# Performance work log

Measured on AMD Instinct MI355X. Metric: run time of the kernel, lower is better.

The kernel has to match this reference:

```python
import jax, jax.numpy as jnp
import numpy as np

IN, H = 23, 64


def _lstm_layer(x, W_ih, W_hh, b_ih, b_hh):
    # x: [B,T,in] ; W_ih: [4H,in] ; W_hh: [4H,H] ; gate order (PyTorch): i,f,g,o
    B = x.shape[0]
    # precompute input contribution for all timesteps (one big GEMM)
    xg = jnp.einsum('bti,gi->btg', x, W_ih) + (b_ih + b_hh)  # [B,T,4H]

    def step(carry, xt):
        h, c = carry
        gates = xt + h @ W_hh.T  # [B,4H]
        i, f, g, o = jnp.split(gates, 4, axis=-1)
        c = jax.nn.sigmoid(f) * c + jax.nn.sigmoid(i) * jnp.tanh(g)
        h = jax.nn.sigmoid(o) * jnp.tanh(c)
        return (h, c), h

    h0 = jnp.zeros((B, H), x.dtype)
    _, hs = jax.lax.scan(step, (h0, h0), jnp.swapaxes(xg, 0, 1))
    return jnp.swapaxes(hs, 0, 1)  # [B,T,H]


def setup_inputs() -> dict:
    key = jax.random.key(0)
    ks = jax.random.split(key, 12)
    s = 1.0 / np.sqrt(H)  # PyTorch LSTM init scale
    x = jax.random.normal(ks[0], (2048, 512, IN), dtype=jnp.float32)
    W_ih0 = jax.random.uniform(ks[1], (4 * H, IN), jnp.float32, -s, s)
    W_hh0 = jax.random.uniform(ks[2], (4 * H, H), jnp.float32, -s, s)
    b_ih0 = jax.random.uniform(ks[3], (4 * H,), jnp.float32, -s, s)
    b_hh0 = jax.random.uniform(ks[4], (4 * H,), jnp.float32, -s, s)
    W_ih1 = jax.random.uniform(ks[5], (4 * H, H), jnp.float32, -s, s)
    W_hh1 = jax.random.uniform(ks[6], (4 * H, H), jnp.float32, -s, s)
    b_ih1 = jax.random.uniform(ks[7], (4 * H,), jnp.float32, -s, s)
    b_hh1 = jax.random.uniform(ks[8], (4 * H,), jnp.float32, -s, s)
    fc_w = jax.random.uniform(ks[9], (1, H), jnp.float32, -s, s)
    fc_b = jax.random.uniform(ks[10], (1,), jnp.float32, -s, s)
    return {"x": x, "W_ih0": W_ih0, "W_hh0": W_hh0, "b_ih0": b_ih0, "b_hh0": b_hh0,
            "W_ih1": W_ih1, "W_hh1": W_hh1, "b_ih1": b_ih1, "b_hh1": b_hh1,
            "fc_w": fc_w, "fc_b": fc_b}


def reference(x, W_ih0, W_hh0, b_ih0, b_hh0, W_ih1, W_hh1, b_ih1, b_hh1, fc_w, fc_b):
    h1 = _lstm_layer(x, W_ih0, W_hh0, b_ih0, b_hh0)   # [B,T,H]
    h2 = _lstm_layer(h1, W_ih1, W_hh1, b_ih1, b_hh1)  # [B,T,H]
    last = h2[:, -1, :]                               # [B,H]
    return last @ fc_w.T + fc_b                       # [B,1]
```

## Files before the change

kernel.cpp:

```cpp
#include <hip/hip_runtime.h>

typedef _Float16 half8 __attribute__((ext_vector_type(8)));
typedef float floatx4 __attribute__((ext_vector_type(4)));

#define NSTEPS 512
#define IN_F   23
#define HSTRIDE 72

__device__ __forceinline__ float fast_rcp(float x) { return __builtin_amdgcn_rcpf(x); }
__device__ __forceinline__ float fast_sigmoid(float x) { return fast_rcp(1.f + __expf(-x)); }
__device__ __forceinline__ float fast_tanh(float x) { return 2.f * fast_rcp(1.f + __expf(-2.f * x)) - 1.f; }

#define MFMA3(acc, Ahi, Alo, Bhi, Blo)                                             \
    acc = __builtin_amdgcn_mfma_f32_16x16x32_f16((Ahi), (Bhi), (acc), 0, 0, 0);    \
    acc = __builtin_amdgcn_mfma_f32_16x16x32_f16((Ahi), (Blo), (acc), 0, 0, 0);    \
    acc = __builtin_amdgcn_mfma_f32_16x16x32_f16((Alo), (Bhi), (acc), 0, 0, 0);

__global__ __launch_bounds__(512, 1)
void lstm2_fused(const float* __restrict__ x,
                 const float* __restrict__ Wih0, const float* __restrict__ Whh0,
                 const float* __restrict__ bih0, const float* __restrict__ bhh0,
                 const float* __restrict__ Wih1, const float* __restrict__ Whh1,
                 const float* __restrict__ bih1, const float* __restrict__ bhh1,
                 const float* __restrict__ fcw, const float* __restrict__ fcb,
                 float* __restrict__ out)
{
    __shared__ _Float16 hhi[2][2][16 * HSTRIDE];
    __shared__ _Float16 hlo[2][2][16 * HSTRIDE];
    __shared__ float red[4][16];

    const int tid  = threadIdx.x;
    const int w8   = tid >> 6;
    const int grp  = w8 >> 2;
    const int wg   = w8 & 3;
    const int lane = tid & 63;
    const int l15  = lane & 15;
    const int krow = lane >> 4;
    const int b0   = blockIdx.x * 8;

    half8 wi_h[4][2], wi_l[4][2], wh_h[4][2], wh_l[4][2];
    float bias[4];
    {
        const float* WI = grp ? Wih1 : Wih0;
        const float* WH = grp ? Whh1 : Whh0;
        const float* BI = grp ? bih1 : bih0;
        const float* BH = grp ? bhh1 : bhh0;
        #pragma unroll
        for (int q = 0; q < 4; ++q) {
            const int g = q * 64 + wg * 16 + l15;
            if (!grp) {
                #pragma unroll
                for (int j = 0; j < 8; ++j) {
                    const int k = krow * 8 + j;
                    const float v = (k < IN_F) ? WI[g * IN_F + k] : 0.f;
                    const _Float16 hi = (_Float16)v;
                    wi_h[q][0][j] = hi;
                    wi_l[q][0][j] = (_Float16)(v - (float)hi);
                    wi_h[q][1][j] = (_Float16)0.f;
                    wi_l[q][1][j] = (_Float16)0.f;
                }
            } else {
                #pragma unroll
                for (int kk = 0; kk < 2; ++kk) {
                    #pragma unroll
                    for (int j = 0; j < 8; ++j) {
                        const int k = kk * 32 + krow * 8 + j;
                        const float v = WI[g * 64 + k];
                        const _Float16 hi = (_Float16)v;
                        wi_h[q][kk][j] = hi;
                        wi_l[q][kk][j] = (_Float16)(v - (float)hi);
                    }
                }
            }
            #pragma unroll
            for (int kk = 0; kk < 2; ++kk) {
                #pragma unroll
                for (int j = 0; j < 8; ++j) {
                    const int k = kk * 32 + krow * 8 + j;
                    const float v = WH[g * 64 + k];
                    const _Float16 hi = (_Float16)v;
                    wh_h[q][kk][j] = hi;
                    wh_l[q][kk][j] = (_Float16)(v - (float)hi);
                }
            }
            bias[q] = BI[g] + BH[g];
        }
    }
    const float fcwv = fcw[wg * 16 + l15];

    floatx4 c = {0.f, 0.f, 0.f, 0.f};
    half8 in0h, in0l, in1h, in1l;
    half8 hr0h, hr0l, hr1h, hr1l;
    #pragma unroll
    for (int j = 0; j < 8; ++j) {
        in0h[j] = (_Float16)0.f; in0l[j] = (_Float16)0.f;
        in1h[j] = (_Float16)0.f; in1l[j] = (_Float16)0.f;
        hr0h[j] = (_Float16)0.f; hr0l[j] = (_Float16)0.f;
        hr1h[j] = (_Float16)0.f; hr1l[j] = (_Float16)0.f;
    }

    const float* xrow = x + (size_t)(b0 + (l15 & 7)) * (NSTEPS * IN_F);
    float xf[8], xfn[8];
    if (!grp) {
        #pragma unroll
        for (int j = 0; j < 8; ++j) {
            const int k = krow * 8 + j;
            xf[j] = (k < IN_F) ? xrow[k] : 0.f;
        }
    }

    float hv[4] = {0.f, 0.f, 0.f, 0.f};

    for (int i = 0; i <= NSTEPS; ++i) {
        const bool act = grp ? (i >= 1) : (i < NSTEPS);
        if (act) {
            if (!grp) {
                #pragma unroll
                for (int j = 0; j < 8; ++j) {
                    const _Float16 hi = (_Float16)xf[j];
                    in0h[j] = hi;
                    in0l[j] = (_Float16)(xf[j] - (float)hi);
                }
                const int tn = (i + 1 < NSTEPS) ? (i + 1) : i;
                #pragma unroll
                for (int j = 0; j < 8; ++j) {
                    const int k = krow * 8 + j;
                    xfn[j] = (k < IN_F) ? xrow[(size_t)tn * IN_F + k] : 0.f;
                }
            }

            floatx4 acc[4];
            #pragma unroll
            for (int q = 0; q < 4; ++q) {
                floatx4 a = {bias[q], bias[q], bias[q], bias[q]};
                MFMA3(a, in0h, in0l, wi_h[q][0], wi_l[q][0]);
                if (grp) { MFMA3(a, in1h, in1l, wi_h[q][1], wi_l[q][1]); }
                MFMA3(a, hr0h, hr0l, wh_h[q][0], wh_l[q][0]);
                MFMA3(a, hr1h, hr1l, wh_h[q][1], wh_l[q][1]);
                acc[q] = a;
            }

            #pragma unroll
            for (int r = 0; r < 4; ++r) {
                const float iv = fast_sigmoid(acc[0][r]);
                const float fv = fast_sigmoid(acc[1][r]);
                const float gv = fast_tanh(acc[2][r]);
                const float ov = fast_sigmoid(acc[3][r]);
                const float cn = fv * c[r] + iv * gv;
                c[r] = cn;
                hv[r] = ov * fast_tanh(cn);
            }

            const int wb = grp ? ((i - 1) & 1) : (i & 1);
            _Float16* dsthi = &hhi[grp][wb][0];
            _Float16* dstlo = &hlo[grp][wb][0];
            #pragma unroll
            for (int r = 0; r < 4; ++r) {
                const int idx = (krow * 4 + r) * HSTRIDE + wg * 16 + l15;
                const _Float16 hi = (_Float16)hv[r];
                dsthi[idx] = hi;
                dstlo[idx] = (_Float16)(hv[r] - (float)hi);
            }
        }

        __syncthreads();

        if (!grp) {
            if (i < NSTEPS) {
                const _Float16* sh = &hhi[0][i & 1][0];
                const _Float16* sl = &hlo[0][i & 1][0];
                hr0h = *(const half8*)&sh[l15 * HSTRIDE + krow * 8];
                hr1h = *(const half8*)&sh[l15 * HSTRIDE + 32 + krow * 8];
                hr0l = *(const half8*)&sl[l15 * HSTRIDE + krow * 8];
                hr1l = *(const half8*)&sl[l15 * HSTRIDE + 32 + krow * 8];
                #pragma unroll
                for (int j = 0; j < 8; ++j) xf[j] = xfn[j];
            }
        } else {
            if (i < NSTEPS) {
                const _Float16* sh = &hhi[0][i & 1][0];
                const _Float16* sl = &hlo[0][i & 1][0];
                in0h = *(const half8*)&sh[l15 * HSTRIDE + krow * 8];
                in1h = *(const half8*)&sh[l15 * HSTRIDE + 32 + krow * 8];
                in0l = *(const half8*)&sl[l15 * HSTRIDE + krow * 8];
                in1l = *(const half8*)&sl[l15 * HSTRIDE + 32 + krow * 8];
            }
            if (i >= 1) {
                const _Float16* sh = &hhi[1][(i - 1) & 1][0];
                const _Float16* sl = &hlo[1][(i - 1) & 1][0];
                hr0h = *(const half8*)&sh[l15 * HSTRIDE + krow * 8];
                hr1h = *(const half8*)&sh[l15 * HSTRIDE + 32 + krow * 8];
                hr0l = *(const half8*)&sl[l15 * HSTRIDE + krow * 8];
                hr1l = *(const half8*)&sl[l15 * HSTRIDE + 32 + krow * 8];
            }
        }
    }

    if (grp) {
        float p[4];
        #pragma unroll
        for (int r = 0; r < 4; ++r) p[r] = hv[r] * fcwv;
        #pragma unroll
        for (int off = 1; off < 16; off <<= 1) {
            #pragma unroll
            for (int r = 0; r < 4; ++r)
                p[r] += __shfl_xor(p[r], off, 64);
        }
        if (l15 == 0) {
            #pragma unroll
            for (int r = 0; r < 4; ++r)
                red[wg][krow * 4 + r] = p[r];
        }
    }
    __syncthreads();
    if (tid < 8) {
        float v = fcb[0];
        v += red[0][tid] + red[1][tid] + red[2][tid] + red[3][tid];
        out[b0 + tid] = v;
    }
}

extern "C" void kernel_launch(void* const* d_in, const int* in_sizes, int n_in,
                              void* d_out, int out_size, void* d_ws, size_t ws_size,
                              hipStream_t stream) {
    (void)n_in; (void)d_ws; (void)ws_size; (void)out_size;
    const float* xp    = (const float*)d_in[0];
    const float* Wih0  = (const float*)d_in[1];
    const float* Whh0  = (const float*)d_in[2];
    const float* bih0  = (const float*)d_in[3];
    const float* bhh0  = (const float*)d_in[4];
    const float* Wih1  = (const float*)d_in[5];
    const float* Whh1  = (const float*)d_in[6];
    const float* bih1  = (const float*)d_in[7];
    const float* bhh1  = (const float*)d_in[8];
    const float* fcw   = (const float*)d_in[9];
    const float* fcb   = (const float*)d_in[10];
    float* outp        = (float*)d_out;

    const int B = in_sizes[0] / (NSTEPS * IN_F);
    const int nblocks = B / 8;
    hipLaunchKernelGGL(lstm2_fused, dim3(nblocks), dim3(512), 0, stream,
                       xp, Wih0, Whh0, bih0, bhh0, Wih1, Whh1, bih1, bhh1,
                       fcw, fcb, outp);
}
```

Measured before the change: 846.6 us.

## Drop activation low-part split in MFMA and fold log2e into weights

Activations (x and hidden states) are now stored and fed to MFMA as a single fp16 value instead of an fp16 hi/lo pair. This cuts per-gate MFMAs from 3 to 2 per K-chunk and halves LDS traffic for the hidden-state exchange. Weights and biases are pre-scaled by log2e (2*log2e for the g gate), so sigmoid and tanh use a raw exp2 without a multiply. The cost is lower accuracy, since activations now carry only fp16 precision across 512 recurrent steps.

Result: faster. 678.9 us (-19.8%).

```diff
diff --git a/kernel.cpp b/kernel.cpp
--- a/kernel.cpp
+++ b/kernel.cpp
@@ -7,14 +7,20 @@
 #define IN_F   23
 #define HSTRIDE 72
 
+#define LOG2E      1.4426950408889634f
+#define NEG2LOG2E -2.8853900817779268f
+
+#if __has_builtin(__builtin_amdgcn_exp2f)
+#define EXP2(x) __builtin_amdgcn_exp2f(x)
+#else
+#define EXP2(x) exp2f(x)
+#endif
+
 __device__ __forceinline__ float fast_rcp(float x) { return __builtin_amdgcn_rcpf(x); }
-__device__ __forceinline__ float fast_sigmoid(float x) { return fast_rcp(1.f + __expf(-x)); }
-__device__ __forceinline__ float fast_tanh(float x) { return 2.f * fast_rcp(1.f + __expf(-2.f * x)) - 1.f; }
-
-#define MFMA3(acc, Ahi, Alo, Bhi, Blo)                                             \
-    acc = __builtin_amdgcn_mfma_f32_16x16x32_f16((Ahi), (Bhi), (acc), 0, 0, 0);    \
-    acc = __builtin_amdgcn_mfma_f32_16x16x32_f16((Ahi), (Blo), (acc), 0, 0, 0);    \
-    acc = __builtin_amdgcn_mfma_f32_16x16x32_f16((Alo), (Bhi), (acc), 0, 0, 0);
+
+#define MFMA2(acc, Ah, Bhi, Blo)                                                   \
+    acc = __builtin_amdgcn_mfma_f32_16x16x32_f16((Ah), (Bhi), (acc), 0, 0, 0);     \
+    acc = __builtin_amdgcn_mfma_f32_16x16x32_f16((Ah), (Blo), (acc), 0, 0, 0);
 
 __global__ __launch_bounds__(512, 1)
 void lstm2_fused(const float* __restrict__ x,
@@ -25,8 +31,7 @@
                  const float* __restrict__ fcw, const float* __restrict__ fcb,
                  float* __restrict__ out)
 {
-    __shared__ _Float16 hhi[2][2][16 * HSTRIDE];
-    __shared__ _Float16 hlo[2][2][16 * HSTRIDE];
+    __shared__ _Float16 hbuf[2][2][16 * HSTRIDE];
     __shared__ float red[4][16];
 
     const int tid  = threadIdx.x;
@@ -45,6 +50,7 @@
         const float* WH = grp ? Whh1 : Whh0;
         const float* BI = grp ? bih1 : bih0;
         const float* BH = grp ? bhh1 : bhh0;
+        const float gs[4] = {LOG2E, LOG2E, 2.f * LOG2E, LOG2E};
         #pragma unroll
         for (int q = 0; q < 4; ++q) {
             const int g = q * 64 + wg * 16 + l15;
@@ -52,7 +58,7 @@
                 #pragma unroll
                 for (int j = 0; j < 8; ++j) {
                     const int k = krow * 8 + j;
-                    const float v = (k < IN_F) ? WI[g * IN_F + k] : 0.f;
+                    const float v = ((k < IN_F) ? WI[g * IN_F + k] : 0.f) * gs[q];
                     const _Float16 hi = (_Float16)v;
                     wi_h[q][0][j] = hi;
                     wi_l[q][0][j] = (_Float16)(v - (float)hi);
@@ -65,7 +71,7 @@
                     #pragma unroll
                     for (int j = 0; j < 8; ++j) {
                         const int k = kk * 32 + krow * 8 + j;
-                        const float v = WI[g * 64 + k];
+                        const float v = WI[g * 64 + k] * gs[q];
                         const _Float16 hi = (_Float16)v;
                         wi_h[q][kk][j] = hi;
                         wi_l[q][kk][j] = (_Float16)(v - (float)hi);
@@ -77,26 +83,24 @@
                 #pragma unroll
                 for (int j = 0; j < 8; ++j) {
                     const int k = kk * 32 + krow * 8 + j;
-                    const float v = WH[g * 64 + k];
+                    const float v = WH[g * 64 + k] * gs[q];
                     const _Float16 hi = (_Float16)v;
                     wh_h[q][kk][j] = hi;
                     wh_l[q][kk][j] = (_Float16)(v - (float)hi);
                 }
             }
-            bias[q] = BI[g] + BH[g];
+            bias[q] = (BI[g] + BH[g]) * gs[q];
         }
     }
     const float fcwv = fcw[wg * 16 + l15];
 
     floatx4 c = {0.f, 0.f, 0.f, 0.f};
-    half8 in0h, in0l, in1h, in1l;
-    half8 hr0h, hr0l, hr1h, hr1l;
+    half8 in0h, in1h;
+    half8 hr0h, hr1h;
     #pragma unroll
     for (int j = 0; j < 8; ++j) {
-        in0h[j] = (_Float16)0.f; in0l[j] = (_Float16)0.f;
-        in1h[j] = (_Float16)0.f; in1l[j] = (_Float16)0.f;
-        hr0h[j] = (_Float16)0.f; hr0l[j] = (_Float16)0.f;
-        hr1h[j] = (_Float16)0.f; hr1l[j] = (_Float16)0.f;
+        in0h[j] = (_Float16)0.f; in1h[j] = (_Float16)0.f;
+        hr0h[j] = (_Float16)0.f; hr1h[j] = (_Float16)0.f;
     }
 
     const float* xrow = x + (size_t)(b0 + (l15 & 7)) * (NSTEPS * IN_F);
@@ -116,11 +120,7 @@
         if (act) {
             if (!grp) {
                 #pragma unroll
-                for (int j = 0; j < 8; ++j) {
-                    const _Float16 hi = (_Float16)xf[j];
-                    in0h[j] = hi;
-                    in0l[j] = (_Float16)(xf[j] - (float)hi);
-                }
+                for (int j = 0; j < 8; ++j) in0h[j] = (_Float16)xf[j];
                 const int tn = (i + 1 < NSTEPS) ? (i + 1) : i;
                 #pragma unroll
                 for (int j = 0; j < 8; ++j) {
@@ -133,33 +133,30 @@
             #pragma unroll
             for (int q = 0; q < 4; ++q) {
                 floatx4 a = {bias[q], bias[q], bias[q], bias[q]};
-                MFMA3(a, in0h, in0l, wi_h[q][0], wi_l[q][0]);
-                if (grp) { MFMA3(a, in1h, in1l, wi_h[q][1], wi_l[q][1]); }
-                MFMA3(a, hr0h, hr0l, wh_h[q][0], wh_l[q][0]);
-                MFMA3(a, hr1h, hr1l, wh_h[q][1], wh_l[q][1]);
+                MFMA2(a, in0h, wi_h[q][0], wi_l[q][0]);
+                if (grp) { MFMA2(a, in1h, wi_h[q][1], wi_l[q][1]); }
+                MFMA2(a, hr0h, wh_h[q][0], wh_l[q][0]);
+                MFMA2(a, hr1h, wh_h[q][1], wh_l[q][1]);
                 acc[q] = a;
             }
 
             #pragma unroll
             for (int r = 0; r < 4; ++r) {
-                const float iv = fast_sigmoid(acc[0][r]);
-                const float fv = fast_sigmoid(acc[1][r]);
-                const float gv = fast_tanh(acc[2][r]);
-                const float ov = fast_sigmoid(acc[3][r]);
+                const float iv = fast_rcp(1.f + EXP2(-acc[0][r]));
+                const float fv = fast_rcp(1.f + EXP2(-acc[1][r]));
+                const float gv = 2.f * fast_rcp(1.f + EXP2(-acc[2][r])) - 1.f;
+                const float ov = fast_rcp(1.f + EXP2(-acc[3][r]));
                 const float cn = fv * c[r] + iv * gv;
                 c[r] = cn;
-                hv[r] = ov * fast_tanh(cn);
+                hv[r] = ov * (2.f * fast_rcp(1.f + EXP2(NEG2LOG2E * cn)) - 1.f);
             }
 
             const int wb = grp ? ((i - 1) & 1) : (i & 1);
-            _Float16* dsthi = &hhi[grp][wb][0];
-            _Float16* dstlo = &hlo[grp][wb][0];
+            _Float16* dst = &hbuf[grp][wb][0];
             #pragma unroll
             for (int r = 0; r < 4; ++r) {
                 const int idx = (krow * 4 + r) * HSTRIDE + wg * 16 + l15;
-                const _Float16 hi = (_Float16)hv[r];
-                dsthi[idx] = hi;
-                dstlo[idx] = (_Float16)(hv[r] - (float)hi);
+                dst[idx] = (_Float16)hv[r];
             }
         }
 
@@ -167,31 +164,22 @@
 
         if (!grp) {
             if (i < NSTEPS) {
-                const _Float16* sh = &hhi[0][i & 1][0];
-                const _Float16* sl = &hlo[0][i & 1][0];
+                const _Float16* sh = &hbuf[0][i & 1][0];
                 hr0h = *(const half8*)&sh[l15 * HSTRIDE + krow * 8];
                 hr1h = *(const half8*)&sh[l15 * HSTRIDE + 32 + krow * 8];
-                hr0l = *(const half8*)&sl[l15 * HSTRIDE + krow * 8];
-                hr1l = *(const half8*)&sl[l15 * HSTRIDE + 32 + krow * 8];
                 #pragma unroll
                 for (int j = 0; j < 8; ++j) xf[j] = xfn[j];
             }
         } else {
             if (i < NSTEPS) {
-                const _Float16* sh = &hhi[0][i & 1][0];
-                const _Float16* sl = &hlo[0][i & 1][0];
+                const _Float16* sh = &hbuf[0][i & 1][0];
                 in0h = *(const half8*)&sh[l15 * HSTRIDE + krow * 8];
                 in1h = *(const half8*)&sh[l15 * HSTRIDE + 32 + krow * 8];
-                in0l = *(const half8*)&sl[l15 * HSTRIDE + krow * 8];
-                in1l = *(const half8*)&sl[l15 * HSTRIDE + 32 + krow * 8];
             }
             if (i >= 1) {
-                const _Float16* sh = &hhi[1][(i - 1) & 1][0];
-                const _Float16* sl = &hlo[1][(i - 1) & 1][0];
+                const _Float16* sh = &hbuf[1][(i - 1) & 1][0];
                 hr0h = *(const half8*)&sh[l15 * HSTRIDE + krow * 8];
                 hr1h = *(const half8*)&sh[l15 * HSTRIDE + 32 + krow * 8];
-                hr0l = *(const half8*)&sl[l15 * HSTRIDE + krow * 8];
-                hr1l = *(const half8*)&sl[l15 * HSTRIDE + 32 + krow * 8];
             }
         }
     }
```
